# Optimization experiments

Hardware: AMD Instinct MI355X
Metric: run time of the kernel (lower is better)

## Reference

```python
import jax, jax.numpy as jnp
import numpy as np

N_NODES = 50000
N_EDGES = 800000


def gcn_conv(x, edge_index, W, b, num_nodes):
    # PyG GCNConv: out = D^-1/2 (A + I) D^-1/2 (X W) + b, with added self-loops.
    xw = x @ W  # [N, F_out]
    src, dst = edge_index[0], edge_index[1]
    loop = jnp.arange(num_nodes, dtype=src.dtype)
    src = jnp.concatenate([src, loop])
    dst = jnp.concatenate([dst, loop])
    # degree (unweighted, after self-loops) on destination nodes
    deg = jax.ops.segment_sum(jnp.ones_like(dst, dtype=xw.dtype), dst,
                              num_segments=num_nodes)
    dinv = jnp.where(deg > 0, jax.lax.rsqrt(deg), 0.0)
    norm = dinv[src] * dinv[dst]  # [E+N]
    msgs = xw[src] * norm[:, None]  # gather + scale
    out = jax.ops.segment_sum(msgs, dst, num_segments=num_nodes)  # scatter-add
    return out + b


def setup_inputs() -> dict:
    key = jax.random.key(0)
    k1, k2, k3, k4 = jax.random.split(key, 4)
    x = jax.random.normal(k1, (N_NODES, 1100), dtype=jnp.float32)
    edge_index = jax.random.randint(k2, (2, N_EDGES), 0, N_NODES, dtype=jnp.int64)
    W1 = jax.random.normal(k3, (512, 256), dtype=jnp.float32) * (1.0 / np.sqrt(512))
    b1 = jnp.zeros((256,), dtype=jnp.float32)
    W2 = jax.random.normal(k4, (256, 128), dtype=jnp.float32) * (1.0 / np.sqrt(256))
    b2 = jnp.zeros((128,), dtype=jnp.float32)
    return {"x": x, "edge_index": edge_index, "W1": W1, "b1": b1,
            "W2": W2, "b2": b2}


def reference(x, edge_index, W1, b1, W2, b2):
    protein_feature = x[:, 588:]  # [N, 512]
    h = gcn_conv(protein_feature, edge_index, W1, b1, N_NODES)
    h = jax.nn.relu(h)
    return gcn_conv(h, edge_index, W2, b2, N_NODES)
```

## Files before the change

### kernel.cpp

```cpp
#include <hip/hip_runtime.h>
#include <hip/hip_bf16.h>
#include <stdint.h>

#define N_NODES 50000
#define N_EDGES 800000
#define CAP 64

typedef __attribute__((ext_vector_type(8))) __bf16 bf16x8;
typedef __attribute__((ext_vector_type(4))) float floatx4;

__device__ __forceinline__ unsigned short f2bf(float f) {
    union { float f; unsigned u; } v; v.f = f;
    unsigned r = v.u + 0x7fffu + ((v.u >> 16) & 1u);
    return (unsigned short)(r >> 16);
}
__device__ __forceinline__ float bf2f(unsigned short h) {
    union { unsigned u; float f; } v; v.u = ((unsigned)h) << 16;
    return v.f;
}

__global__ __launch_bounds__(256) void bucket_fill_kernel(
    const int* __restrict__ src, const int* __restrict__ dst,
    unsigned* __restrict__ cnt, int* __restrict__ bucket, int nE)
{
    int i = blockIdx.x * blockDim.x + threadIdx.x;
    if (i < nE) {
        unsigned d = (unsigned)dst[i];
        unsigned s = (unsigned)src[i];
        if (d < N_NODES && s < N_NODES) {
            unsigned slot = atomicAdd(&cnt[d], 1u);
            if (slot < CAP) bucket[(size_t)d * CAP + slot] = (int)s;
        }
    }
}

__global__ __launch_bounds__(256) void split_w_both_kernel(
    const float* __restrict__ W1, unsigned short* __restrict__ T1h, unsigned short* __restrict__ T1l,
    const float* __restrict__ W2, unsigned short* __restrict__ T2h, unsigned short* __restrict__ T2l)
{
    const int n1 = 512 * 256;
    const int n2 = 256 * 128;
    int i = blockIdx.x * blockDim.x + threadIdx.x;
    if (i < n1) {
        int k = i >> 8;
        int n = i & 255;
        float w = W1[i];
        unsigned short hi = f2bf(w);
        unsigned short lo = f2bf(w - bf2f(hi));
        T1h[(size_t)n * 512 + k] = hi;
        T1l[(size_t)n * 512 + k] = lo;
    } else if (i < n1 + n2) {
        int j = i - n1;
        int k = j >> 7;
        int n = j & 127;
        float w = W2[j];
        unsigned short hi = f2bf(w);
        unsigned short lo = f2bf(w - bf2f(hi));
        T2h[(size_t)n * 256 + k] = hi;
        T2l[(size_t)n * 256 + k] = lo;
    }
}

#define GBM 64
#define GBK 32

__device__ __forceinline__ int chunk_off(int row, int q) {
    return row * 32 + ((q ^ ((row >> 1) & 3)) << 3);
}

template<bool AFP32, int BN>
__global__ __launch_bounds__(256, 2) void gemm_mfma_kernel(
    const float* __restrict__ Afp, int lda,
    const unsigned short* __restrict__ Ah, const unsigned short* __restrict__ Al, int apitch,
    const unsigned short* __restrict__ BTh, const unsigned short* __restrict__ BTl,
    const unsigned* __restrict__ cnt, float* __restrict__ Y,
    int M, int K, int N)
{
    constexpr int WCOLS = BN / 4;
    constexpr int NJ    = WCOLS / 16;
    constexpr int BCPT  = BN / 64;

    __shared__ unsigned short sAh[GBM * GBK];
    __shared__ unsigned short sAl[GBM * GBK];
    __shared__ unsigned short sBh[BN * GBK];
    __shared__ unsigned short sBl[BN * GBK];

    const int t    = threadIdx.x;
    const int bm   = blockIdx.x * GBM;
    const int bn   = 0;
    const int w    = t >> 6;
    const int lane = t & 63;
    const int ml   = lane & 15;
    const int quad = lane >> 4;

    const int asr = t >> 2;
    const int aq  = t & 3;
    const int bsr = (BN == 256) ? t : (t >> 1);
    const int bq0 = (BN == 256) ? 0 : ((t & 1) * 2);

    floatx4 zero4 = {0.f, 0.f, 0.f, 0.f};
    floatx4 acc[4][NJ];
    #pragma unroll
    for (int i = 0; i < 4; ++i)
        #pragma unroll
        for (int j = 0; j < NJ; ++j) acc[i][j] = zero4;

    for (int k0 = 0; k0 < K; k0 += GBK) {
        {
            int gr = bm + asr;
            if (AFP32) {
                float4 v0, v1;
                if (gr < M) {
                    const float* ap = Afp + (size_t)gr * lda + k0 + aq * 8;
                    v0 = *(const float4*)(ap);
                    v1 = *(const float4*)(ap + 4);
                } else {
                    v0 = make_float4(0.f,0.f,0.f,0.f);
                    v1 = make_float4(0.f,0.f,0.f,0.f);
                }
                union { unsigned short us[8]; uint4 v; } ph, pl;
                float f[8] = {v0.x, v0.y, v0.z, v0.w, v1.x, v1.y, v1.z, v1.w};
                #pragma unroll
                for (int e = 0; e < 8; ++e) {
                    unsigned short hi = f2bf(f[e]);
                    ph.us[e] = hi;
                    pl.us[e] = f2bf(f[e] - bf2f(hi));
                }
                int off = chunk_off(asr, aq);
                *(uint4*)&sAh[off] = ph.v;
                *(uint4*)&sAl[off] = pl.v;
            } else {
                uint4 vh, vl;
                if (gr < M) {
                    vh = *(const uint4*)(Ah + (size_t)gr * apitch + k0 + aq * 8);
                    vl = *(const uint4*)(Al + (size_t)gr * apitch + k0 + aq * 8);
                } else {
                    vh = make_uint4(0,0,0,0);
                    vl = make_uint4(0,0,0,0);
                }
                int off = chunk_off(asr, aq);
                *(uint4*)&sAh[off] = vh;
                *(uint4*)&sAl[off] = vl;
            }
        }
        {
            const unsigned short* bh = BTh + (size_t)(bn + bsr) * K + k0;
            const unsigned short* bl = BTl + (size_t)(bn + bsr) * K + k0;
            #pragma unroll
            for (int c = 0; c < BCPT; ++c) {
                int q = bq0 + c;
                uint4 vh = *(const uint4*)(bh + q * 8);
                uint4 vl = *(const uint4*)(bl + q * 8);
                int off = chunk_off(bsr, q);
                *(uint4*)&sBh[off] = vh;
                *(uint4*)&sBl[off] = vl;
            }
        }
        __syncthreads();

        bf16x8 fAh[4], fAl[4];
        #pragma unroll
        for (int i = 0; i < 4; ++i) {
            int row = i * 16 + ml;
            int off = chunk_off(row, quad);
            fAh[i] = *(const bf16x8*)&sAh[off];
            fAl[i] = *(const bf16x8*)&sAl[off];
        }

        #pragma unroll
        for (int j = 0; j < NJ; ++j) {
            int nrow = w * WCOLS + j * 16 + ml;
            int off = chunk_off(nrow, quad);
            bf16x8 fBh = *(const bf16x8*)&sBh[off];
            bf16x8 fBl = *(const bf16x8*)&sBl[off];
            #pragma unroll
            for (int i = 0; i < 4; ++i) {
                floatx4 c = acc[i][j];
                c = __builtin_amdgcn_mfma_f32_16x16x32_bf16(fAh[i], fBh, c, 0, 0, 0);
                c = __builtin_amdgcn_mfma_f32_16x16x32_bf16(fAl[i], fBh, c, 0, 0, 0);
                c = __builtin_amdgcn_mfma_f32_16x16x32_bf16(fAh[i], fBl, c, 0, 0, 0);
                acc[i][j] = c;
            }
        }
        __syncthreads();
    }

    #pragma unroll
    for (int i = 0; i < 4; ++i) {
        int rb = bm + i * 16 + quad * 4;
        float sc[4];
        #pragma unroll
        for (int r = 0; r < 4; ++r)
            sc[r] = (rb + r < M) ? rsqrtf((float)(cnt[rb + r] + 1u)) : 0.f;
        #pragma unroll
        for (int j = 0; j < NJ; ++j) {
            int col = w * WCOLS + j * 16 + ml;
            #pragma unroll
            for (int r = 0; r < 4; ++r) {
                int grow = rb + r;
                if (grow < M) Y[(size_t)grow * N + col] = acc[i][j][r] * sc[r];
            }
        }
    }
}

__global__ __launch_bounds__(256) void aggregate256_kernel(
    const float* __restrict__ Y, const int* __restrict__ bucket,
    const unsigned* __restrict__ cnt, const float* __restrict__ bias,
    unsigned short* __restrict__ Hh, unsigned short* __restrict__ Hl)
{
    const int v  = blockIdx.x * 4 + (threadIdx.x >> 6);
    const int f0 = (threadIdx.x & 63) * 4;

    float4 a0 = *(const float4*)(Y + (size_t)v * 256 + f0);
    float4 a1 = make_float4(0.f,0.f,0.f,0.f);
    float4 a2 = make_float4(0.f,0.f,0.f,0.f);
    float4 a3 = make_float4(0.f,0.f,0.f,0.f);

    const int* bp = bucket + (size_t)v * CAP;
    const unsigned deg = min(cnt[v], (unsigned)CAP);
    unsigned j = 0;
    for (; j + 4 <= deg; j += 4) {
        int u0 = bp[j + 0];
        int u1 = bp[j + 1];
        int u2 = bp[j + 2];
        int u3 = bp[j + 3];
        float4 m0 = *(const float4*)(Y + (size_t)u0 * 256 + f0);
        float4 m1 = *(const float4*)(Y + (size_t)u1 * 256 + f0);
        float4 m2 = *(const float4*)(Y + (size_t)u2 * 256 + f0);
        float4 m3 = *(const float4*)(Y + (size_t)u3 * 256 + f0);
        a0.x += m0.x; a0.y += m0.y; a0.z += m0.z; a0.w += m0.w;
        a1.x += m1.x; a1.y += m1.y; a1.z += m1.z; a1.w += m1.w;
        a2.x += m2.x; a2.y += m2.y; a2.z += m2.z; a2.w += m2.w;
        a3.x += m3.x; a3.y += m3.y; a3.z += m3.z; a3.w += m3.w;
    }
    for (; j < deg; ++j) {
        float4 m = *(const float4*)(Y + (size_t)bp[j] * 256 + f0);
        a0.x += m.x; a0.y += m.y; a0.z += m.z; a0.w += m.w;
    }
    float sx = (a0.x + a1.x) + (a2.x + a3.x);
    float sy = (a0.y + a1.y) + (a2.y + a3.y);
    float sz = (a0.z + a1.z) + (a2.z + a3.z);
    float sw = (a0.w + a1.w) + (a2.w + a3.w);

    float dv = rsqrtf((float)(cnt[v] + 1u));
    float4 b = *(const float4*)(bias + f0);
    float r[4];
    r[0] = fmaxf(sx * dv + b.x, 0.f);
    r[1] = fmaxf(sy * dv + b.y, 0.f);
    r[2] = fmaxf(sz * dv + b.z, 0.f);
    r[3] = fmaxf(sw * dv + b.w, 0.f);

    union { unsigned short us[4]; ushort4 v4; } ph, pl;
    #pragma unroll
    for (int e = 0; e < 4; ++e) {
        unsigned short hi = f2bf(r[e]);
        ph.us[e] = hi;
        pl.us[e] = f2bf(r[e] - bf2f(hi));
    }
    *(ushort4*)(Hh + (size_t)v * 256 + f0) = ph.v4;
    *(ushort4*)(Hl + (size_t)v * 256 + f0) = pl.v4;
}

__global__ __launch_bounds__(256) void aggregate128_kernel(
    const float* __restrict__ Y, const int* __restrict__ bucket,
    const unsigned* __restrict__ cnt, const float* __restrict__ bias,
    float* __restrict__ out)
{
    const int v  = blockIdx.x * 8 + (threadIdx.x >> 5);
    const int f0 = (threadIdx.x & 31) * 4;

    float4 a0 = *(const float4*)(Y + (size_t)v * 128 + f0);
    float4 a1 = make_float4(0.f,0.f,0.f,0.f);
    float4 a2 = make_float4(0.f,0.f,0.f,0.f);
    float4 a3 = make_float4(0.f,0.f,0.f,0.f);

    const int* bp = bucket + (size_t)v * CAP;
    const unsigned deg = min(cnt[v], (unsigned)CAP);
    unsigned j = 0;
    for (; j + 4 <= deg; j += 4) {
        int u0 = bp[j + 0];
        int u1 = bp[j + 1];
        int u2 = bp[j + 2];
        int u3 = bp[j + 3];
        float4 m0 = *(const float4*)(Y + (size_t)u0 * 128 + f0);
        float4 m1 = *(const float4*)(Y + (size_t)u1 * 128 + f0);
        float4 m2 = *(const float4*)(Y + (size_t)u2 * 128 + f0);
        float4 m3 = *(const float4*)(Y + (size_t)u3 * 128 + f0);
        a0.x += m0.x; a0.y += m0.y; a0.z += m0.z; a0.w += m0.w;
        a1.x += m1.x; a1.y += m1.y; a1.z += m1.z; a1.w += m1.w;
        a2.x += m2.x; a2.y += m2.y; a2.z += m2.z; a2.w += m2.w;
        a3.x += m3.x; a3.y += m3.y; a3.z += m3.z; a3.w += m3.w;
    }
    for (; j < deg; ++j) {
        float4 m = *(const float4*)(Y + (size_t)bp[j] * 128 + f0);
        a0.x += m.x; a0.y += m.y; a0.z += m.z; a0.w += m.w;
    }
    float sx = (a0.x + a1.x) + (a2.x + a3.x);
    float sy = (a0.y + a1.y) + (a2.y + a3.y);
    float sz = (a0.z + a1.z) + (a2.z + a3.z);
    float sw = (a0.w + a1.w) + (a2.w + a3.w);

    float dv = rsqrtf((float)(cnt[v] + 1u));
    float4 b = *(const float4*)(bias + f0);
    float4 r;
    r.x = sx * dv + b.x;
    r.y = sy * dv + b.y;
    r.z = sz * dv + b.z;
    r.w = sw * dv + b.w;
    *(float4*)(out + (size_t)v * 128 + f0) = r;
}

extern "C" void kernel_launch(void* const* d_in, const int* in_sizes, int n_in,
                              void* d_out, int out_size, void* d_ws, size_t ws_size,
                              hipStream_t stream)
{
    const float* x  = (const float*)d_in[0];
    const int*   ei = (const int*)d_in[1];
    const float* W1 = (const float*)d_in[2];
    const float* b1 = (const float*)d_in[3];
    const float* W2 = (const float*)d_in[4];
    const float* b2 = (const float*)d_in[5];
    float*       out = (float*)d_out;

    const int* e_src = ei;
    const int* e_dst = ei + N_EDGES;

    char* ws = (char*)d_ws;
    size_t o = 0;
    auto carve = [&](size_t bytes) -> char* {
        char* p = ws + o;
        o = (o + bytes + 511) & ~(size_t)511;
        return p;
    };
    unsigned*       cnt    = (unsigned*)carve((size_t)N_NODES * 4);
    int*            bucket = (int*)carve((size_t)N_NODES * CAP * 4);
    unsigned short* WT1h   = (unsigned short*)carve((size_t)512 * 256 * 2);
    unsigned short* WT1l   = (unsigned short*)carve((size_t)512 * 256 * 2);
    unsigned short* WT2h   = (unsigned short*)carve((size_t)256 * 128 * 2);
    unsigned short* WT2l   = (unsigned short*)carve((size_t)256 * 128 * 2);
    float*          y      = (float*)carve((size_t)N_NODES * 256 * 4);
    unsigned short* Hh     = (unsigned short*)carve((size_t)N_NODES * 256 * 2);
    unsigned short* Hl     = (unsigned short*)carve((size_t)N_NODES * 256 * 2);
    (void)ws_size;

    hipMemsetAsync(cnt, 0, (size_t)N_NODES * 4, stream);

    bucket_fill_kernel<<<(N_EDGES + 255) / 256, 256, 0, stream>>>(e_src, e_dst, cnt, bucket, N_EDGES);

    split_w_both_kernel<<<(512 * 256 + 256 * 128 + 255) / 256, 256, 0, stream>>>(
        W1, WT1h, WT1l, W2, WT2h, WT2l);

    {
        dim3 grid((N_NODES + GBM - 1) / GBM, 1);
        gemm_mfma_kernel<true, 256><<<grid, 256, 0, stream>>>(
            x + 588, 1100, nullptr, nullptr, 0, WT1h, WT1l, cnt, y,
            N_NODES, 512, 256);
    }
    aggregate256_kernel<<<N_NODES / 4, 256, 0, stream>>>(y, bucket, cnt, b1, Hh, Hl);

    {
        dim3 grid((N_NODES + GBM - 1) / GBM, 1);
        gemm_mfma_kernel<false, 128><<<grid, 256, 0, stream>>>(
            nullptr, 0, Hh, Hl, 256, WT2h, WT2l, cnt, y,
            N_NODES, 256, 128);
    }
    aggregate128_kernel<<<N_NODES / 8, 256, 0, stream>>>(y, bucket, cnt, b2, out);
}
```

Measured before the change: 618.4 us.

## Enlarge GEMM M-tile to 128 with 2x2 warp grid and register prefetch

Doubles the GEMM block tile in M from 64 to 128 rows and arranges the four waves as a 2x2 grid, so each B tile loaded into shared memory is reused across twice as many rows. It also adds register-staged prefetching: the next K-tile's global loads are issued before the MFMA work on the current tile and written to shared memory afterwards. This cuts B-matrix global traffic and overlaps load latency with compute. In exchange it needs more registers per thread (larger accumulator array plus prefetch buffers), which may reduce occupancy under the 2-blocks-per-CU launch bound, and it halves the number of blocks.

```diff
diff --git a/kernel.cpp b/kernel.cpp
--- a/kernel.cpp
+++ b/kernel.cpp
@@ -61,7 +61,7 @@
     }
 }
 
-#define GBM 64
+#define GBM 128
 #define GBK 32
 
 __device__ __forceinline__ int chunk_off(int row, int q) {
@@ -76,9 +76,9 @@
     const unsigned* __restrict__ cnt, float* __restrict__ Y,
     int M, int K, int N)
 {
-    constexpr int WCOLS = BN / 4;
+    constexpr int WCOLS = BN / 2;
     constexpr int NJ    = WCOLS / 16;
-    constexpr int BCPT  = BN / 64;
+    constexpr int BROWS = BN / 128;
 
     __shared__ unsigned short sAh[GBM * GBK];
     __shared__ unsigned short sAl[GBM * GBK];
@@ -87,81 +87,114 @@
 
     const int t    = threadIdx.x;
     const int bm   = blockIdx.x * GBM;
-    const int bn   = 0;
     const int w    = t >> 6;
     const int lane = t & 63;
+    const int wx   = w & 1;
+    const int wy   = w >> 1;
     const int ml   = lane & 15;
     const int quad = lane >> 4;
 
-    const int asr = t >> 2;
-    const int aq  = t & 3;
-    const int bsr = (BN == 256) ? t : (t >> 1);
-    const int bq0 = (BN == 256) ? 0 : ((t & 1) * 2);
-
-    floatx4 zero4 = {0.f, 0.f, 0.f, 0.f};
-    floatx4 acc[4][NJ];
-    #pragma unroll
-    for (int i = 0; i < 4; ++i)
-        #pragma unroll
-        for (int j = 0; j < NJ; ++j) acc[i][j] = zero4;
-
-    for (int k0 = 0; k0 < K; k0 += GBK) {
-        {
-            int gr = bm + asr;
+    const int sr = t >> 1;
+    const int q0 = (t & 1) * 2;
+
+    float4 pa[2][2];
+    uint4  pah[2], pal[2];
+    uint4  pbh[BROWS][2], pbl[BROWS][2];
+
+    const int gr = bm + sr;
+    const bool arow_ok = (gr < M);
+
+    auto load_tile = [&](int k0) {
+        if (AFP32) {
+            #pragma unroll
+            for (int c = 0; c < 2; ++c) {
+                if (arow_ok) {
+                    const float* ap = Afp + (size_t)gr * lda + k0 + (q0 + c) * 8;
+                    pa[c][0] = *(const float4*)(ap);
+                    pa[c][1] = *(const float4*)(ap + 4);
+                } else {
+                    pa[c][0] = make_float4(0.f,0.f,0.f,0.f);
+                    pa[c][1] = make_float4(0.f,0.f,0.f,0.f);
+                }
+            }
+        } else {
+            #pragma unroll
+            for (int c = 0; c < 2; ++c) {
+                if (arow_ok) {
+                    pah[c] = *(const uint4*)(Ah + (size_t)gr * apitch + k0 + (q0 + c) * 8);
+                    pal[c] = *(const uint4*)(Al + (size_t)gr * apitch + k0 + (q0 + c) * 8);
+                } else {
+                    pah[c] = make_uint4(0,0,0,0);
+                    pal[c] = make_uint4(0,0,0,0);
+                }
+            }
+        }
+        #pragma unroll
+        for (int r = 0; r < BROWS; ++r) {
+            int nr = sr + r * 128;
+            const unsigned short* bh = BTh + (size_t)nr * K + k0;
+            const unsigned short* bl = BTl + (size_t)nr * K + k0;
+            #pragma unroll
+            for (int c = 0; c < 2; ++c) {
+                pbh[r][c] = *(const uint4*)(bh + (q0 + c) * 8);
+                pbl[r][c] = *(const uint4*)(bl + (q0 + c) * 8);
+            }
+        }
+    };
+
+    auto write_tile = [&]() {
+        #pragma unroll
+        for (int c = 0; c < 2; ++c) {
+            int off = chunk_off(sr, q0 + c);
             if (AFP32) {
-                float4 v0, v1;
-                if (gr < M) {
-                    const float* ap = Afp + (size_t)gr * lda + k0 + aq * 8;
-                    v0 = *(const float4*)(ap);
-                    v1 = *(const float4*)(ap + 4);
-                } else {
-                    v0 = make_float4(0.f,0.f,0.f,0.f);
-                    v1 = make_float4(0.f,0.f,0.f,0.f);
-                }
                 union { unsigned short us[8]; uint4 v; } ph, pl;
-                float f[8] = {v0.x, v0.y, v0.z, v0.w, v1.x, v1.y, v1.z, v1.w};
+                float f[8] = {pa[c][0].x, pa[c][0].y, pa[c][0].z, pa[c][0].w,
+                              pa[c][1].x, pa[c][1].y, pa[c][1].z, pa[c][1].w};
                 #pragma unroll
                 for (int e = 0; e < 8; ++e) {
                     unsigned short hi = f2bf(f[e]);
                     ph.us[e] = hi;
                     pl.us[e] = f2bf(f[e] - bf2f(hi));
                 }
-                int off = chunk_off(asr, aq);
                 *(uint4*)&sAh[off] = ph.v;
                 *(uint4*)&sAl[off] = pl.v;
             } else {
-                uint4 vh, vl;
-                if (gr < M) {
-                    vh = *(const uint4*)(Ah + (size_t)gr * apitch + k0 + aq * 8);
-                    vl = *(const uint4*)(Al + (size_t)gr * apitch + k0 + aq * 8);
-                } else {
-                    vh = make_uint4(0,0,0,0);
-                    vl = make_uint4(0,0,0,0);
-                }
-                int off = chunk_off(asr, aq);
-                *(uint4*)&sAh[off] = vh;
-                *(uint4*)&sAl[off] = vl;
-            }
-        }
-        {
-            const unsigned short* bh = BTh + (size_t)(bn + bsr) * K + k0;
-            const unsigned short* bl = BTl + (size_t)(bn + bsr) * K + k0;
-            #pragma unroll
-            for (int c = 0; c < BCPT; ++c) {
-                int q = bq0 + c;
-                uint4 vh = *(const uint4*)(bh + q * 8);
-                uint4 vl = *(const uint4*)(bl + q * 8);
-                int off = chunk_off(bsr, q);
-                *(uint4*)&sBh[off] = vh;
-                *(uint4*)&sBl[off] = vl;
-            }
-        }
-        __syncthreads();
+                *(uint4*)&sAh[off] = pah[c];
+                *(uint4*)&sAl[off] = pal[c];
+            }
+        }
+        #pragma unroll
+        for (int r = 0; r < BROWS; ++r) {
+            int nr = sr + r * 128;
+            #pragma unroll
+            for (int c = 0; c < 2; ++c) {
+                int off = chunk_off(nr, q0 + c);
+                *(uint4*)&sBh[off] = pbh[r][c];
+                *(uint4*)&sBl[off] = pbl[r][c];
+            }
+        }
+    };
+
+    floatx4 zero4 = {0.f, 0.f, 0.f, 0.f};
+    floatx4 acc[4][NJ];
+    #pragma unroll
+    for (int i = 0; i < 4; ++i)
+        #pragma unroll
+        for (int j = 0; j < NJ; ++j) acc[i][j] = zero4;
+
+    const int NT = K / GBK;
+
+    load_tile(0);
+    write_tile();
+    __syncthreads();
+
+    for (int tt = 0; tt < NT; ++tt) {
+        if (tt + 1 < NT) load_tile((tt + 1) * GBK);
 
         bf16x8 fAh[4], fAl[4];
         #pragma unroll
         for (int i = 0; i < 4; ++i) {
-            int row = i * 16 + ml;
+            int row = wy * 64 + i * 16 + ml;
             int off = chunk_off(row, quad);
             fAh[i] = *(const bf16x8*)&sAh[off];
             fAl[i] = *(const bf16x8*)&sAl[off];
@@ -169,7 +202,7 @@
 
         #pragma unroll
         for (int j = 0; j < NJ; ++j) {
-            int nrow = w * WCOLS + j * 16 + ml;
+            int nrow = wx * WCOLS + j * 16 + ml;
             int off = chunk_off(nrow, quad);
             bf16x8 fBh = *(const bf16x8*)&sBh[off];
             bf16x8 fBl = *(const bf16x8*)&sBl[off];
@@ -183,18 +216,23 @@
             }
         }
         __syncthreads();
+
+        if (tt + 1 < NT) {
+            write_tile();
+            __syncthreads();
+        }
     }
 
     #pragma unroll
     for (int i = 0; i < 4; ++i) {
-        int rb = bm + i * 16 + quad * 4;
+        int rb = bm + wy * 64 + i * 16 + quad * 4;
         float sc[4];
         #pragma unroll
         for (int r = 0; r < 4; ++r)
             sc[r] = (rb + r < M) ? rsqrtf((float)(cnt[rb + r] + 1u)) : 0.f;
         #pragma unroll
         for (int j = 0; j < NJ; ++j) {
-            int col = w * WCOLS + j * 16 + ml;
+            int col = wx * WCOLS + j * 16 + ml;
             #pragma unroll
             for (int r = 0; r < 4; ++r) {
                 int grow = rb + r;
```

After: 660.5 us. 6.8% more time.

## Pre-tile operands into swizzled LDS images and load via global_load_lds

Applied to the files above, without the earlier changes.

Adds a split_x pre-pass that converts x into bf16 hi/lo tiles already laid out in the swizzled shared-memory image format. The weight split and the layer-1 aggregate now write that same tiled format, and row count is padded to a multiple of 128. The GEMM grows to 128-row tiles with a 2x2 wave layout and fills shared memory with direct global-to-LDS DMA instead of register staging and in-kernel conversion. The aim is to cut conversion work and load overhead inside the GEMM, at the cost of an extra pass over x and a larger workspace.

```diff
diff --git a/kernel.cpp b/kernel.cpp
--- a/kernel.cpp
+++ b/kernel.cpp
@@ -5,6 +5,10 @@
 #define N_NODES 50000
 #define N_EDGES 800000
 #define CAP 64
+#define MP 50048
+
+#define AS1 __attribute__((address_space(1)))
+#define AS3 __attribute__((address_space(3)))
 
 typedef __attribute__((ext_vector_type(8))) __bf16 bf16x8;
 typedef __attribute__((ext_vector_type(4))) float floatx4;
@@ -17,6 +21,10 @@
 __device__ __forceinline__ float bf2f(unsigned short h) {
     union { unsigned u; float f; } v; v.u = ((unsigned)h) << 16;
     return v.f;
+}
+
+__device__ __forceinline__ int img_off(int row, int q) {
+    return row * 32 + ((q ^ ((row >> 1) & 3)) << 3);
 }
 
 __global__ __launch_bounds__(256) void bucket_fill_kernel(
@@ -34,6 +42,35 @@
     }
 }
 
+__global__ __launch_bounds__(256) void split_x_kernel(
+    const float* __restrict__ x, unsigned short* __restrict__ Xh, unsigned short* __restrict__ Xl)
+{
+    int id = blockIdx.x * 256 + threadIdx.x;
+    int gr = id >> 6;
+    int c  = id & 63;
+    int kt = c >> 2, q = c & 3;
+    int lr = gr & 127;
+    size_t off = ((size_t)((gr >> 7) * 16 + kt)) * 4096 + img_off(lr, q);
+    union { unsigned short us[8]; uint4 v; } ph, pl;
+    if (gr < N_NODES) {
+        const float* ap = x + (size_t)gr * 1100 + 588 + kt * 32 + q * 8;
+        float4 v0 = *(const float4*)ap;
+        float4 v1 = *(const float4*)(ap + 4);
+        float f[8] = {v0.x, v0.y, v0.z, v0.w, v1.x, v1.y, v1.z, v1.w};
+        #pragma unroll
+        for (int e = 0; e < 8; ++e) {
+            unsigned short hi = f2bf(f[e]);
+            ph.us[e] = hi;
+            pl.us[e] = f2bf(f[e] - bf2f(hi));
+        }
+    } else {
+        ph.v = make_uint4(0, 0, 0, 0);
+        pl.v = make_uint4(0, 0, 0, 0);
+    }
+    *(uint4*)&Xh[off] = ph.v;
+    *(uint4*)&Xl[off] = pl.v;
+}
+
 __global__ __launch_bounds__(256) void split_w_both_kernel(
     const float* __restrict__ W1, unsigned short* __restrict__ T1h, unsigned short* __restrict__ T1l,
     const float* __restrict__ W2, unsigned short* __restrict__ T2h, unsigned short* __restrict__ T2l)
@@ -42,61 +79,45 @@
     const int n2 = 256 * 128;
     int i = blockIdx.x * blockDim.x + threadIdx.x;
     if (i < n1) {
-        int k = i >> 8;
-        int n = i & 255;
+        int k = i >> 8, n = i & 255;
         float w = W1[i];
-        unsigned short hi = f2bf(w);
-        unsigned short lo = f2bf(w - bf2f(hi));
-        T1h[(size_t)n * 512 + k] = hi;
-        T1l[(size_t)n * 512 + k] = lo;
+        unsigned short hi = f2bf(w), lo = f2bf(w - bf2f(hi));
+        size_t off = (size_t)(k >> 5) * 8192 + img_off(n, (k >> 3) & 3) + (k & 7);
+        T1h[off] = hi; T1l[off] = lo;
     } else if (i < n1 + n2) {
         int j = i - n1;
-        int k = j >> 7;
-        int n = j & 127;
+        int k = j >> 7, n = j & 127;
         float w = W2[j];
-        unsigned short hi = f2bf(w);
-        unsigned short lo = f2bf(w - bf2f(hi));
-        T2h[(size_t)n * 256 + k] = hi;
-        T2l[(size_t)n * 256 + k] = lo;
-    }
-}
-
-#define GBM 64
-#define GBK 32
-
-__device__ __forceinline__ int chunk_off(int row, int q) {
-    return row * 32 + ((q ^ ((row >> 1) & 3)) << 3);
-}
-
-template<bool AFP32, int BN>
+        unsigned short hi = f2bf(w), lo = f2bf(w - bf2f(hi));
+        size_t off = (size_t)(k >> 5) * 4096 + img_off(n, (k >> 3) & 3) + (k & 7);
+        T2h[off] = hi; T2l[off] = lo;
+    }
+}
+
+template<int BN>
 __global__ __launch_bounds__(256, 2) void gemm_mfma_kernel(
-    const float* __restrict__ Afp, int lda,
-    const unsigned short* __restrict__ Ah, const unsigned short* __restrict__ Al, int apitch,
+    const unsigned short* __restrict__ Ah, const unsigned short* __restrict__ Al,
     const unsigned short* __restrict__ BTh, const unsigned short* __restrict__ BTl,
     const unsigned* __restrict__ cnt, float* __restrict__ Y,
     int M, int K, int N)
 {
-    constexpr int WCOLS = BN / 4;
+    constexpr int WCOLS = BN / 2;
     constexpr int NJ    = WCOLS / 16;
-    constexpr int BCPT  = BN / 64;
-
-    __shared__ unsigned short sAh[GBM * GBK];
-    __shared__ unsigned short sAl[GBM * GBK];
-    __shared__ unsigned short sBh[BN * GBK];
-    __shared__ unsigned short sBl[BN * GBK];
+    constexpr int BIMG  = BN * 32;
+
+    __shared__ __align__(16) unsigned short sAh[128 * 32];
+    __shared__ __align__(16) unsigned short sAl[128 * 32];
+    __shared__ __align__(16) unsigned short sBh[BIMG];
+    __shared__ __align__(16) unsigned short sBl[BIMG];
 
     const int t    = threadIdx.x;
-    const int bm   = blockIdx.x * GBM;
-    const int bn   = 0;
+    const int bm   = blockIdx.x * 128;
     const int w    = t >> 6;
     const int lane = t & 63;
+    const int wx   = w & 1;
+    const int wy   = w >> 1;
     const int ml   = lane & 15;
     const int quad = lane >> 4;
-
-    const int asr = t >> 2;
-    const int aq  = t & 3;
-    const int bsr = (BN == 256) ? t : (t >> 1);
-    const int bq0 = (BN == 256) ? 0 : ((t & 1) * 2);
 
     floatx4 zero4 = {0.f, 0.f, 0.f, 0.f};
     floatx4 acc[4][NJ];
@@ -105,81 +126,47 @@
         #pragma unroll
         for (int j = 0; j < NJ; ++j) acc[i][j] = zero4;
 
-    for (int k0 = 0; k0 < K; k0 += GBK) {
-        {
-            int gr = bm + asr;
-            if (AFP32) {
-                float4 v0, v1;
-                if (gr < M) {
-                    const float* ap = Afp + (size_t)gr * lda + k0 + aq * 8;
-                    v0 = *(const float4*)(ap);
-                    v1 = *(const float4*)(ap + 4);
-                } else {
-                    v0 = make_float4(0.f,0.f,0.f,0.f);
-                    v1 = make_float4(0.f,0.f,0.f,0.f);
-                }
-                union { unsigned short us[8]; uint4 v; } ph, pl;
-                float f[8] = {v0.x, v0.y, v0.z, v0.w, v1.x, v1.y, v1.z, v1.w};
-                #pragma unroll
-                for (int e = 0; e < 8; ++e) {
-                    unsigned short hi = f2bf(f[e]);
-                    ph.us[e] = hi;
-                    pl.us[e] = f2bf(f[e] - bf2f(hi));
-                }
-                int off = chunk_off(asr, aq);
-                *(uint4*)&sAh[off] = ph.v;
-                *(uint4*)&sAl[off] = pl.v;
-            } else {
-                uint4 vh, vl;
-                if (gr < M) {
-                    vh = *(const uint4*)(Ah + (size_t)gr * apitch + k0 + aq * 8);
-                    vl = *(const uint4*)(Al + (size_t)gr * apitch + k0 + aq * 8);
-                } else {
-                    vh = make_uint4(0,0,0,0);
-                    vl = make_uint4(0,0,0,0);
-                }
-                int off = chunk_off(asr, aq);
-                *(uint4*)&sAh[off] = vh;
-                *(uint4*)&sAl[off] = vl;
-            }
-        }
-        {
-            const unsigned short* bh = BTh + (size_t)(bn + bsr) * K + k0;
-            const unsigned short* bl = BTl + (size_t)(bn + bsr) * K + k0;
-            #pragma unroll
-            for (int c = 0; c < BCPT; ++c) {
-                int q = bq0 + c;
-                uint4 vh = *(const uint4*)(bh + q * 8);
-                uint4 vl = *(const uint4*)(bl + q * 8);
-                int off = chunk_off(bsr, q);
-                *(uint4*)&sBh[off] = vh;
-                *(uint4*)&sBl[off] = vl;
-            }
+    const int NKT = K >> 5;
+    for (int kt = 0; kt < NKT; ++kt) {
+        const unsigned short* ah = Ah + ((size_t)(blockIdx.x * NKT + kt)) * 4096;
+        const unsigned short* al = Al + ((size_t)(blockIdx.x * NKT + kt)) * 4096;
+        const unsigned short* bh = BTh + (size_t)kt * BIMG;
+        const unsigned short* bl = BTl + (size_t)kt * BIMG;
+
+        #pragma unroll
+        for (int c = 0; c < 2; ++c) {
+            int eo = c * 2048 + t * 8;
+            __builtin_amdgcn_global_load_lds((const AS1 void*)(ah + eo), (AS3 void*)&sAh[eo], 16, 0, 0);
+            __builtin_amdgcn_global_load_lds((const AS1 void*)(al + eo), (AS3 void*)&sAl[eo], 16, 0, 0);
+        }
+        #pragma unroll
+        for (int c = 0; c < BN / 64; ++c) {
+            int eo = c * 2048 + t * 8;
+            __builtin_amdgcn_global_load_lds((const AS1 void*)(bh + eo), (AS3 void*)&sBh[eo], 16, 0, 0);
+            __builtin_amdgcn_global_load_lds((const AS1 void*)(bl + eo), (AS3 void*)&sBl[eo], 16, 0, 0);
         }
         __syncthreads();
 
         bf16x8 fAh[4], fAl[4];
         #pragma unroll
         for (int i = 0; i < 4; ++i) {
-            int row = i * 16 + ml;
-            int off = chunk_off(row, quad);
+            int off = img_off(wy * 64 + i * 16 + ml, quad);
             fAh[i] = *(const bf16x8*)&sAh[off];
             fAl[i] = *(const bf16x8*)&sAl[off];
         }
 
         #pragma unroll
         for (int j = 0; j < NJ; ++j) {
-            int nrow = w * WCOLS + j * 16 + ml;
-            int off = chunk_off(nrow, quad);
+            int off = img_off(wx * WCOLS + j * 16 + ml, quad);
             bf16x8 fBh = *(const bf16x8*)&sBh[off];
             bf16x8 fBl = *(const bf16x8*)&sBl[off];
             #pragma unroll
             for (int i = 0; i < 4; ++i) {
-                floatx4 c = acc[i][j];
-                c = __builtin_amdgcn_mfma_f32_16x16x32_bf16(fAh[i], fBh, c, 0, 0, 0);
-                c = __builtin_amdgcn_mfma_f32_16x16x32_bf16(fAl[i], fBh, c, 0, 0, 0);
-                c = __builtin_amdgcn_mfma_f32_16x16x32_bf16(fAh[i], fBl, c, 0, 0, 0);
-                acc[i][j] = c;
+                floatx4 c2 = acc[i][j];
+                c2 = __builtin_amdgcn_mfma_f32_16x16x32_bf16(fAh[i], fBh, c2, 0, 0, 0);
+                c2 = __builtin_amdgcn_mfma_f32_16x16x32_bf16(fAl[i], fBh, c2, 0, 0, 0);
+                c2 = __builtin_amdgcn_mfma_f32_16x16x32_bf16(fAh[i], fBl, c2, 0, 0, 0);
+                acc[i][j] = c2;
             }
         }
         __syncthreads();
@@ -187,14 +174,14 @@
 
     #pragma unroll
     for (int i = 0; i < 4; ++i) {
-        int rb = bm + i * 16 + quad * 4;
+        int rb = bm + wy * 64 + i * 16 + quad * 4;
         float sc[4];
         #pragma unroll
         for (int r = 0; r < 4; ++r)
             sc[r] = (rb + r < M) ? rsqrtf((float)(cnt[rb + r] + 1u)) : 0.f;
         #pragma unroll
         for (int j = 0; j < NJ; ++j) {
-            int col = w * WCOLS + j * 16 + ml;
+            int col = wx * WCOLS + j * 16 + ml;
             #pragma unroll
             for (int r = 0; r < 4; ++r) {
                 int grow = rb + r;
@@ -211,6 +198,16 @@
 {
     const int v  = blockIdx.x * 4 + (threadIdx.x >> 6);
     const int f0 = (threadIdx.x & 63) * 4;
+    const int lr = v & 127;
+    const size_t hoff = ((size_t)((v >> 7) * 8 + (f0 >> 5))) * 4096
+                      + (size_t)img_off(lr, (f0 >> 3) & 3) + (f0 & 7);
+
+    if (v >= N_NODES) {
+        ushort4 z = make_ushort4(0, 0, 0, 0);
+        *(ushort4*)&Hh[hoff] = z;
+        *(ushort4*)&Hl[hoff] = z;
+        return;
+    }
 
     float4 a0 = *(const float4*)(Y + (size_t)v * 256 + f0);
     float4 a1 = make_float4(0.f,0.f,0.f,0.f);
@@ -258,8 +255,8 @@
         ph.us[e] = hi;
         pl.us[e] = f2bf(r[e] - bf2f(hi));
     }
-    *(ushort4*)(Hh + (size_t)v * 256 + f0) = ph.v4;
-    *(ushort4*)(Hl + (size_t)v * 256 + f0) = pl.v4;
+    *(ushort4*)&Hh[hoff] = ph.v4;
+    *(ushort4*)&Hl[hoff] = pl.v4;
 }
 
 __global__ __launch_bounds__(256) void aggregate128_kernel(
@@ -339,9 +336,11 @@
     unsigned short* WT1l   = (unsigned short*)carve((size_t)512 * 256 * 2);
     unsigned short* WT2h   = (unsigned short*)carve((size_t)256 * 128 * 2);
     unsigned short* WT2l   = (unsigned short*)carve((size_t)256 * 128 * 2);
+    unsigned short* Xh     = (unsigned short*)carve((size_t)MP * 512 * 2);
+    unsigned short* Xl     = (unsigned short*)carve((size_t)MP * 512 * 2);
     float*          y      = (float*)carve((size_t)N_NODES * 256 * 4);
-    unsigned short* Hh     = (unsigned short*)carve((size_t)N_NODES * 256 * 2);
-    unsigned short* Hl     = (unsigned short*)carve((size_t)N_NODES * 256 * 2);
+    unsigned short* Hh     = (unsigned short*)carve((size_t)MP * 256 * 2);
+    unsigned short* Hl     = (unsigned short*)carve((size_t)MP * 256 * 2);
     (void)ws_size;
 
     hipMemsetAsync(cnt, 0, (size_t)N_NODES * 4, stream);
@@ -350,20 +349,15 @@
 
     split_w_both_kernel<<<(512 * 256 + 256 * 128 + 255) / 256, 256, 0, stream>>>(
         W1, WT1h, WT1l, W2, WT2h, WT2l);
-
-    {
-        dim3 grid((N_NODES + GBM - 1) / GBM, 1);
-        gemm_mfma_kernel<true, 256><<<grid, 256, 0, stream>>>(
-            x + 588, 1100, nullptr, nullptr, 0, WT1h, WT1l, cnt, y,
-            N_NODES, 512, 256);
-    }
-    aggregate256_kernel<<<N_NODES / 4, 256, 0, stream>>>(y, bucket, cnt, b1, Hh, Hl);
-
-    {
-        dim3 grid((N_NODES + GBM - 1) / GBM, 1);
-        gemm_mfma_kernel<false, 128><<<grid, 256, 0, stream>>>(
-            nullptr, 0, Hh, Hl, 256, WT2h, WT2l, cnt, y,
-            N_NODES, 256, 128);
-    }
+    split_x_kernel<<<MP / 4, 256, 0, stream>>>(x, Xh, Xl);
+
+    gemm_mfma_kernel<256><<<MP / 128, 256, 0, stream>>>(
+        Xh, Xl, WT1h, WT1l, cnt, y, N_NODES, 512, 256);
+
+    aggregate256_kernel<<<MP / 4, 256, 0, stream>>>(y, bucket, cnt, b1, Hh, Hl);
+
+    gemm_mfma_kernel<128><<<MP / 128, 256, 0, stream>>>(
+        Hh, Hl, WT2h, WT2l, cnt, y, N_NODES, 256, 128);
+
     aggregate128_kernel<<<N_NODES / 8, 256, 0, stream>>>(y, bucket, cnt, b2, out);
 }
```

After: 595.5 us. -3.7%, faster.
